# Kernel optimization log

Measured on AMD Instinct MI355X. Metric: run time of the kernel, lower is better.

## Reference

```python
import jax, jax.numpy as jnp
import numpy as np

FP8_MAX = 448.0   # torch.finfo(float8_e4m3fn).max
BLK = 128         # block_size = [128, 128] for weights; [1, 128] for activations
E, H, I, T, TOPK = 8, 2048, 1408, 512, 2
FP8 = jnp.float8_e4m3fn


def fp8_round(x):
    """Round-trip through float8_e4m3fn (simulates .to(float8_e4m3fn))."""
    return jnp.clip(x, -FP8_MAX, FP8_MAX).astype(FP8).astype(jnp.float32)


def setup_inputs() -> dict:
    key = jax.random.key(0)
    ks = jax.random.split(key, 7)
    hidden_states = jax.random.normal(ks[0], (T, H), jnp.float32)
    top_k_index = jax.random.randint(ks[1], (T, TOPK), 0, E)
    top_k_weights = jax.random.uniform(ks[2], (T, TOPK), jnp.float32)
    # FP8 weight codes (stored as fp32 values exactly representable in e4m3fn)
    gate_up_proj = fp8_round(jax.random.normal(ks[3], (E, 2 * I, H), jnp.float32))
    gate_up_proj_scale_inv = jax.random.uniform(ks[4], (E, (2 * I) // BLK, H // BLK), jnp.float32, 1e-4, 1e-2)
    down_proj = fp8_round(jax.random.normal(ks[5], (E, H, I), jnp.float32))
    down_proj_scale_inv = jax.random.uniform(ks[6], (E, H // BLK, I // BLK), jnp.float32, 1e-4, 1e-2)
    return {
        "hidden_states": hidden_states,
        "top_k_index": top_k_index,
        "top_k_weights": top_k_weights,
        "gate_up_proj": gate_up_proj,
        "gate_up_proj_scale_inv": gate_up_proj_scale_inv,
        "down_proj": down_proj,
        "down_proj_scale_inv": down_proj_scale_inv,
    }


def dequant_weight(wq, s):
    # wq: [E, N, K] fp8 codes; s: [E, N//BLK, K//BLK] per-128x128-block scale_inv
    e, n, k = wq.shape
    wb = wq.reshape(e, n // BLK, BLK, k // BLK, BLK)
    return (wb * s[:, :, None, :, None]).reshape(e, n, k)


def quant_dequant_act(x):
    # dynamic per-(row, 128-block) fp8 activation quantization, then dequant
    shp = x.shape
    xb = x.reshape(shp[:-1] + (shp[-1] // BLK, BLK))
    amax = jnp.max(jnp.abs(xb), axis=-1, keepdims=True)
    scale = jnp.maximum(amax, 1e-12) / FP8_MAX
    q = fp8_round(xb / scale)
    return (q * scale).reshape(shp)


def reference(hidden_states, top_k_index, top_k_weights, gate_up_proj,
              gate_up_proj_scale_inv, down_proj, down_proj_scale_inv):
    w_gu = dequant_weight(gate_up_proj, gate_up_proj_scale_inv)  # [E, 2I, H]
    w_d = dequant_weight(down_proj, down_proj_scale_inv)         # [E, H, I]
    # activation quantization is per-token-block, so unrouted tokens are
    # unaffected; dense per-expert compute + combine-weight mask equals the
    # original gather/scatter loop exactly (unrouted contributions weight 0).
    x = quant_dequant_act(hidden_states)                         # [T, H]
    gate_up = jnp.einsum('th,enh->etn', x, w_gu)                 # [E, T, 2I]
    gate, up = jnp.split(gate_up, 2, axis=-1)
    h = jax.nn.silu(gate) * up                                   # [E, T, I]
    h = quant_dequant_act(h)
    down = jnp.einsum('eti,ehi->eth', h, w_d)                    # [E, T, H]
    # combine[t, e] = sum over top-k slots routing token t to expert e
    combine = jnp.sum(jax.nn.one_hot(top_k_index, E, dtype=top_k_weights.dtype)
                      * top_k_weights[..., None], axis=1)        # [T, E]
    out = jnp.einsum('eth,te->th', down, combine)
    return out.astype(hidden_states.dtype)
```

## Files before the change

kernel.cpp:

```cpp
#include <hip/hip_runtime.h>
#include <math.h>

#define NE 8
#define HD 2048
#define ID 1408
#define NT 512
#define NENT 1024
#define FP8MAX 448.0f

typedef __attribute__((ext_vector_type(4))) float floatx4;

__device__ __forceinline__ floatx4 fzero4() {
    floatx4 z; z.x = 0.f; z.y = 0.f; z.z = 0.f; z.w = 0.f; return z;
}

#define OFF_OFFS  0
#define OFF_TOK   1024
#define OFF_WGT   8192
#define OFF_XS    16384
#define OFF_XQ    65536
#define OFF_HS    (2*1024*1024)
#define OFF_HQ    (2*1024*1024 + 65536)
#define OFF_H32   (4*1024*1024)

#define LDA 136

__global__ void route_kernel(const int* __restrict__ tki,
                             const float* __restrict__ tkw,
                             int* __restrict__ offs,
                             int* __restrict__ tok,
                             float* __restrict__ wgt) {
    __shared__ int cnt[NE];
    __shared__ int cur[NE];
    __shared__ int base[NE + 1];
    int tid = threadIdx.x;
    if (tid < NE) { cnt[tid] = 0; cur[tid] = 0; }
    __syncthreads();
    int e = tki[tid];
    atomicAdd(&cnt[e], 1);
    __syncthreads();
    if (tid == 0) {
        int s = 0;
        for (int i = 0; i < NE; i++) { base[i] = s; s += cnt[i]; }
        base[NE] = s;
    }
    __syncthreads();
    int pos = atomicAdd(&cur[e], 1);
    int j = base[e] + pos;
    tok[j] = tid >> 1;
    wgt[j] = tkw[tid];
    if (tid <= NE) offs[tid] = base[tid];
}

__global__ void quant_x_kernel(const float* __restrict__ x,
                               unsigned char* __restrict__ xq,
                               float* __restrict__ xs) {
    int wid = (blockIdx.x * 256 + threadIdx.x) >> 6;
    int lane = threadIdx.x & 63;
    int t = wid >> 4;
    int b = wid & 15;
    const float2 v = *(const float2*)(x + (long)t * HD + b * 128 + lane * 2);
    float am = fmaxf(fabsf(v.x), fabsf(v.y));
    #pragma unroll
    for (int m = 32; m; m >>= 1) am = fmaxf(am, __shfl_xor(am, m));
    float scale = fmaxf(am, 1e-12f) / FP8MAX;
    int p = __builtin_amdgcn_cvt_pk_fp8_f32(v.x / scale, v.y / scale, 0, false);
    *(unsigned short*)(xq + (long)t * HD + b * 128 + lane * 2) =
        (unsigned short)(p & 0xffff);
    if (lane == 0) xs[t * 16 + b] = scale;
}

__global__ void quant_h_kernel(const float* __restrict__ h32,
                               unsigned char* __restrict__ hq,
                               float* __restrict__ hs) {
    int wid = (blockIdx.x * 256 + threadIdx.x) >> 6;
    int lane = threadIdx.x & 63;
    int j = wid / 11;
    int b = wid - j * 11;
    const float2 v = *(const float2*)(h32 + (long)j * ID + b * 128 + lane * 2);
    float am = fmaxf(fabsf(v.x), fabsf(v.y));
    #pragma unroll
    for (int m = 32; m; m >>= 1) am = fmaxf(am, __shfl_xor(am, m));
    float scale = fmaxf(am, 1e-12f) / FP8MAX;
    int p = __builtin_amdgcn_cvt_pk_fp8_f32(v.x / scale, v.y / scale, 0, false);
    *(unsigned short*)(hq + (long)j * ID + b * 128 + lane * 2) =
        (unsigned short)(p & 0xffff);
    if (lane == 0) hs[j * 11 + b] = scale;
}

__global__ __launch_bounds__(256) void gemm1_kernel(
    const unsigned char* __restrict__ xq,
    const float* __restrict__ xs,
    const float* __restrict__ wgu,
    const float* __restrict__ sgu,
    const int* __restrict__ offs,
    const int* __restrict__ tok,
    float* __restrict__ h32) {
    int e = blockIdx.z;
    int mt = blockIdx.y;
    int jb = blockIdx.x;
    int o0 = offs[e], o1 = offs[e + 1];
    int ne = o1 - o0;
    int m0 = mt * 256;
    if (m0 >= ne) return;
    int rem = ne - m0;

    __shared__ __align__(16) unsigned char Asm[256 * LDA];
    __shared__ __align__(16) unsigned char Bsm[64 * LDA];
    __shared__ float sxa[256 * 16];
    __shared__ int tokL[256];

    int tid = threadIdx.x;
    {
        int j = o0 + m0 + tid;
        if (j >= o1) j = o0;
        tokL[tid] = tok[j];
    }
    __syncthreads();
    {
        const float4* s = (const float4*)(xs + tokL[tid] * 16);
        float4 a0 = s[0], a1 = s[1], a2 = s[2], a3 = s[3];
        float4* d = (float4*)(sxa + tid * 16);
        d[0] = a0; d[1] = a1; d[2] = a2; d[3] = a3;
    }

    int wave = tid >> 6;
    int lane = tid & 63;
    int lr = lane & 15;
    int lq = lane >> 4;

    const unsigned char* aptr = xq + (long)tokL[tid] * HD;
    int br = tid >> 2, bq = tid & 3;
    long bn = (br < 32) ? (long)(jb * 32 + br)
                        : (long)(1408 + jb * 32 + (br - 32));
    const float* bptr = wgu + ((long)e * 2816 + bn) * 2048;
    const float* sgp = sgu + (e * 22 + (jb >> 2)) * 16;
    const float* sup = sgu + (e * 22 + 11 + (jb >> 2)) * 16;

    floatx4 facc[16];
    #pragma unroll
    for (int i = 0; i < 16; i++) facc[i] = fzero4();

    for (int kb = 0; kb < 16; kb++) {
        {
            const uint4* src = (const uint4*)(aptr + kb * 128);
            uint4 av[8];
            #pragma unroll
            for (int i = 0; i < 8; i++) av[i] = src[i];
            #pragma unroll
            for (int i = 0; i < 8; i++)
                *(uint4*)(&Asm[tid * LDA + i * 16]) = av[i];
        }
        {
            const float4* src = (const float4*)(bptr + kb * 128 + bq * 32);
            unsigned int pk[8];
            #pragma unroll
            for (int g = 0; g < 8; g++) {
                float4 f = src[g];
                int p = __builtin_amdgcn_cvt_pk_fp8_f32(f.x, f.y, 0, false);
                p = __builtin_amdgcn_cvt_pk_fp8_f32(f.z, f.w, p, true);
                pk[g] = (unsigned int)p;
            }
            *(uint4*)(&Bsm[br * LDA + bq * 32]) =
                make_uint4(pk[0], pk[1], pk[2], pk[3]);
            *(uint4*)(&Bsm[br * LDA + bq * 32 + 16]) =
                make_uint4(pk[4], pk[5], pk[6], pk[7]);
        }
        __syncthreads();
        floatx4 cacc[16];
        #pragma unroll
        for (int i = 0; i < 16; i++) cacc[i] = fzero4();
        #pragma unroll
        for (int ks = 0; ks < 4; ks++) {
            long a[4], b[4];
            #pragma unroll
            for (int mi = 0; mi < 4; mi++)
                a[mi] = *(const long*)(&Asm[(wave * 64 + mi * 16 + lr) * LDA + ks * 32 + lq * 8]);
            #pragma unroll
            for (int ni = 0; ni < 4; ni++)
                b[ni] = *(const long*)(&Bsm[(ni * 16 + lr) * LDA + ks * 32 + lq * 8]);
            #pragma unroll
            for (int mi = 0; mi < 4; mi++)
                #pragma unroll
                for (int ni = 0; ni < 4; ni++)
                    cacc[mi * 4 + ni] = __builtin_amdgcn_mfma_f32_16x16x32_fp8_fp8(
                        a[mi], b[ni], cacc[mi * 4 + ni], 0, 0, 0);
        }
        float sg = sgp[kb];
        float su = sup[kb];
        #pragma unroll
        for (int mi = 0; mi < 4; mi++) {
            #pragma unroll
            for (int reg = 0; reg < 4; reg++) {
                float sx = sxa[(wave * 64 + mi * 16 + lq * 4 + reg) * 16 + kb];
                #pragma unroll
                for (int ni = 0; ni < 4; ni++) {
                    float sw = (ni < 2) ? sg : su;
                    facc[mi * 4 + ni][reg] += cacc[mi * 4 + ni][reg] * (sw * sx);
                }
            }
        }
        __syncthreads();
    }

    #pragma unroll
    for (int mi = 0; mi < 4; mi++) {
        #pragma unroll
        for (int ni = 0; ni < 2; ni++) {
            #pragma unroll
            for (int reg = 0; reg < 4; reg++) {
                int r = wave * 64 + mi * 16 + lq * 4 + reg;
                if (r < rem) {
                    float g = facc[mi * 4 + ni][reg];
                    float u = facc[mi * 4 + ni + 2][reg];
                    float hval = (g / (1.0f + expf(-g))) * u;
                    h32[(long)(o0 + m0 + r) * ID + jb * 32 + ni * 16 + lr] = hval;
                }
            }
        }
    }
}

__global__ __launch_bounds__(256) void gemm2_kernel(
    const unsigned char* __restrict__ hq,
    const float* __restrict__ hs,
    const float* __restrict__ wd,
    const float* __restrict__ sd,
    const int* __restrict__ offs,
    const int* __restrict__ tok,
    const float* __restrict__ wgt,
    float* __restrict__ out) {
    int e = blockIdx.z;
    int mt = blockIdx.y;
    int jb = blockIdx.x;
    int o0 = offs[e], o1 = offs[e + 1];
    int ne = o1 - o0;
    int m0 = mt * 256;
    if (m0 >= ne) return;
    int rem = ne - m0;

    __shared__ __align__(16) unsigned char Asm[256 * LDA];
    __shared__ __align__(16) unsigned char Bsm[64 * LDA];
    __shared__ float sha[256 * 12];
    __shared__ int tokL[256];
    __shared__ float wgtL[256];

    int tid = threadIdx.x;
    int jent;
    {
        int j = o0 + m0 + tid;
        int valid = j < o1;
        if (!valid) j = o0;
        jent = j;
        tokL[tid] = tok[j];
        wgtL[tid] = valid ? wgt[j] : 0.0f;
    }
    {
        const float* s = hs + jent * 11;
        #pragma unroll
        for (int k = 0; k < 11; k++) sha[tid * 12 + k] = s[k];
    }

    int wave = tid >> 6;
    int lane = tid & 63;
    int lr = lane & 15;
    int lq = lane >> 4;

    const unsigned char* aptr = hq + (long)jent * ID;
    int br = tid >> 2, bq = tid & 3;
    const float* bptr = wd + ((long)e * 2048 + jb * 64 + br) * 1408;
    const float* sdp = sd + (e * 16 + (jb >> 1)) * 11;

    floatx4 facc[16];
    #pragma unroll
    for (int i = 0; i < 16; i++) facc[i] = fzero4();

    for (int kb = 0; kb < 11; kb++) {
        {
            const uint4* src = (const uint4*)(aptr + kb * 128);
            uint4 av[8];
            #pragma unroll
            for (int i = 0; i < 8; i++) av[i] = src[i];
            #pragma unroll
            for (int i = 0; i < 8; i++)
                *(uint4*)(&Asm[tid * LDA + i * 16]) = av[i];
        }
        {
            const float4* src = (const float4*)(bptr + kb * 128 + bq * 32);
            unsigned int pk[8];
            #pragma unroll
            for (int g = 0; g < 8; g++) {
                float4 f = src[g];
                int p = __builtin_amdgcn_cvt_pk_fp8_f32(f.x, f.y, 0, false);
                p = __builtin_amdgcn_cvt_pk_fp8_f32(f.z, f.w, p, true);
                pk[g] = (unsigned int)p;
            }
            *(uint4*)(&Bsm[br * LDA + bq * 32]) =
                make_uint4(pk[0], pk[1], pk[2], pk[3]);
            *(uint4*)(&Bsm[br * LDA + bq * 32 + 16]) =
                make_uint4(pk[4], pk[5], pk[6], pk[7]);
        }
        __syncthreads();
        floatx4 cacc[16];
        #pragma unroll
        for (int i = 0; i < 16; i++) cacc[i] = fzero4();
        #pragma unroll
        for (int ks = 0; ks < 4; ks++) {
            long a[4], b[4];
            #pragma unroll
            for (int mi = 0; mi < 4; mi++)
                a[mi] = *(const long*)(&Asm[(wave * 64 + mi * 16 + lr) * LDA + ks * 32 + lq * 8]);
            #pragma unroll
            for (int ni = 0; ni < 4; ni++)
                b[ni] = *(const long*)(&Bsm[(ni * 16 + lr) * LDA + ks * 32 + lq * 8]);
            #pragma unroll
            for (int mi = 0; mi < 4; mi++)
                #pragma unroll
                for (int ni = 0; ni < 4; ni++)
                    cacc[mi * 4 + ni] = __builtin_amdgcn_mfma_f32_16x16x32_fp8_fp8(
                        a[mi], b[ni], cacc[mi * 4 + ni], 0, 0, 0);
        }
        float sw = sdp[kb];
        #pragma unroll
        for (int mi = 0; mi < 4; mi++) {
            #pragma unroll
            for (int reg = 0; reg < 4; reg++) {
                float sh = sha[(wave * 64 + mi * 16 + lq * 4 + reg) * 12 + kb];
                #pragma unroll
                for (int ni = 0; ni < 4; ni++)
                    facc[mi * 4 + ni][reg] += cacc[mi * 4 + ni][reg] * (sw * sh);
            }
        }
        __syncthreads();
    }

    #pragma unroll
    for (int mi = 0; mi < 4; mi++) {
        #pragma unroll
        for (int ni = 0; ni < 4; ni++) {
            #pragma unroll
            for (int reg = 0; reg < 4; reg++) {
                int r = wave * 64 + mi * 16 + lq * 4 + reg;
                if (r < rem) {
                    float v = facc[mi * 4 + ni][reg] * wgtL[r];
                    atomicAdd(out + (long)tokL[r] * HD + jb * 64 + ni * 16 + lr, v);
                }
            }
        }
    }
}

extern "C" void kernel_launch(void* const* d_in, const int* in_sizes, int n_in,
                              void* d_out, int out_size, void* d_ws, size_t ws_size,
                              hipStream_t stream) {
    (void)in_sizes; (void)n_in; (void)out_size; (void)ws_size;
    const float* x   = (const float*)d_in[0];
    const int*   tki = (const int*)d_in[1];
    const float* tkw = (const float*)d_in[2];
    const float* wgu = (const float*)d_in[3];
    const float* sgu = (const float*)d_in[4];
    const float* wd  = (const float*)d_in[5];
    const float* sd  = (const float*)d_in[6];
    float* out = (float*)d_out;
    char* ws = (char*)d_ws;

    int*   offs = (int*)(ws + OFF_OFFS);
    int*   tok  = (int*)(ws + OFF_TOK);
    float* wgt  = (float*)(ws + OFF_WGT);
    float* xs   = (float*)(ws + OFF_XS);
    unsigned char* xq = (unsigned char*)(ws + OFF_XQ);
    float* hs   = (float*)(ws + OFF_HS);
    unsigned char* hq = (unsigned char*)(ws + OFF_HQ);
    float* h32  = (float*)(ws + OFF_H32);

    hipMemsetAsync(d_out, 0, (size_t)NT * HD * sizeof(float), stream);
    route_kernel<<<1, 1024, 0, stream>>>(tki, tkw, offs, tok, wgt);
    quant_x_kernel<<<2048, 256, 0, stream>>>(x, xq, xs);
    gemm1_kernel<<<dim3(44, 4, NE), 256, 0, stream>>>(xq, xs, wgu, sgu, offs, tok, h32);
    quant_h_kernel<<<2816, 256, 0, stream>>>(h32, hq, hs);
    gemm2_kernel<<<dim3(32, 4, NE), 256, 0, stream>>>(hq, hs, wd, sd, offs, tok, wgt, out);
}
```

Measured before the change: 423.7 us.

## Pre-convert fp32 weights to fp8 once per call and prefetch next K tile

```diff
diff --git a/kernel.cpp b/kernel.cpp
--- a/kernel.cpp
+++ b/kernel.cpp
@@ -22,6 +22,9 @@
 #define OFF_HS    (2*1024*1024)
 #define OFF_HQ    (2*1024*1024 + 65536)
 #define OFF_H32   (4*1024*1024)
+#define OFF_WGU8  (10*1024*1024)
+#define OFF_WD8   (OFF_WGU8 + 46137344)
+#define WS_NEED   ((size_t)OFF_WD8 + 23068672)
 
 #define LDA 136
 
@@ -52,6 +55,25 @@
     if (tid <= NE) offs[tid] = base[tid];
 }
 
+__global__ __launch_bounds__(256) void conv_w_kernel(
+    const float* __restrict__ wgu, const float* __restrict__ wd,
+    unsigned char* __restrict__ wgu8, unsigned char* __restrict__ wd8) {
+    const long N1 = 11534336;
+    const long N2 = 5767168;
+    long stride = (long)gridDim.x * 256;
+    for (long i = (long)blockIdx.x * 256 + threadIdx.x; i < N1 + N2; i += stride) {
+        const float4* src;
+        unsigned char* dst;
+        long j;
+        if (i < N1) { src = (const float4*)wgu; dst = wgu8; j = i; }
+        else        { src = (const float4*)wd;  dst = wd8;  j = i - N1; }
+        float4 f = src[j];
+        int p = __builtin_amdgcn_cvt_pk_fp8_f32(f.x, f.y, 0, false);
+        p = __builtin_amdgcn_cvt_pk_fp8_f32(f.z, f.w, p, true);
+        *(unsigned int*)(dst + j * 4) = (unsigned int)p;
+    }
+}
+
 __global__ void quant_x_kernel(const float* __restrict__ x,
                                unsigned char* __restrict__ xq,
                                float* __restrict__ xs) {
@@ -88,10 +110,11 @@
     if (lane == 0) hs[j * 11 + b] = scale;
 }
 
+template<int WFP8>
 __global__ __launch_bounds__(256) void gemm1_kernel(
     const unsigned char* __restrict__ xq,
     const float* __restrict__ xs,
-    const float* __restrict__ wgu,
+    const void* __restrict__ wguv,
     const float* __restrict__ sgu,
     const int* __restrict__ offs,
     const int* __restrict__ tok,
@@ -133,7 +156,8 @@
     int br = tid >> 2, bq = tid & 3;
     long bn = (br < 32) ? (long)(jb * 32 + br)
                         : (long)(1408 + jb * 32 + (br - 32));
-    const float* bptr = wgu + ((long)e * 2816 + bn) * 2048;
+    const unsigned char* bptr8 = WFP8 ? (const unsigned char*)wguv + ((long)e * 2816 + bn) * 2048 : nullptr;
+    const float* bptrf = WFP8 ? nullptr : (const float*)wguv + ((long)e * 2816 + bn) * 2048;
     const float* sgp = sgu + (e * 22 + (jb >> 2)) * 16;
     const float* sup = sgu + (e * 22 + 11 + (jb >> 2)) * 16;
 
@@ -141,22 +165,38 @@
     #pragma unroll
     for (int i = 0; i < 16; i++) facc[i] = fzero4();
 
+    uint4 aP[8];
+    uint4 bP8[2];
+    float4 bPf[8];
+
+    auto loadAB = [&](int kb) {
+        const uint4* asrc = (const uint4*)(aptr + kb * 128);
+        #pragma unroll
+        for (int i = 0; i < 8; i++) aP[i] = asrc[i];
+        if (WFP8) {
+            const uint4* bsrc = (const uint4*)(bptr8 + kb * 128 + bq * 32);
+            bP8[0] = bsrc[0];
+            bP8[1] = bsrc[1];
+        } else {
+            const float4* bsrc = (const float4*)(bptrf + kb * 128 + bq * 32);
+            #pragma unroll
+            for (int g = 0; g < 8; g++) bPf[g] = bsrc[g];
+        }
+    };
+    loadAB(0);
+
     for (int kb = 0; kb < 16; kb++) {
-        {
-            const uint4* src = (const uint4*)(aptr + kb * 128);
-            uint4 av[8];
-            #pragma unroll
-            for (int i = 0; i < 8; i++) av[i] = src[i];
-            #pragma unroll
-            for (int i = 0; i < 8; i++)
-                *(uint4*)(&Asm[tid * LDA + i * 16]) = av[i];
-        }
-        {
-            const float4* src = (const float4*)(bptr + kb * 128 + bq * 32);
+        #pragma unroll
+        for (int i = 0; i < 8; i++)
+            *(uint4*)(&Asm[tid * LDA + i * 16]) = aP[i];
+        if (WFP8) {
+            *(uint4*)(&Bsm[br * LDA + bq * 32]) = bP8[0];
+            *(uint4*)(&Bsm[br * LDA + bq * 32 + 16]) = bP8[1];
+        } else {
             unsigned int pk[8];
             #pragma unroll
             for (int g = 0; g < 8; g++) {
-                float4 f = src[g];
+                float4 f = bPf[g];
                 int p = __builtin_amdgcn_cvt_pk_fp8_f32(f.x, f.y, 0, false);
                 p = __builtin_amdgcn_cvt_pk_fp8_f32(f.z, f.w, p, true);
                 pk[g] = (unsigned int)p;
@@ -167,6 +207,7 @@
                 make_uint4(pk[4], pk[5], pk[6], pk[7]);
         }
         __syncthreads();
+        if (kb < 15) loadAB(kb + 1);
         floatx4 cacc[16];
         #pragma unroll
         for (int i = 0; i < 16; i++) cacc[i] = fzero4();
@@ -221,10 +262,11 @@
     }
 }
 
+template<int WFP8>
 __global__ __launch_bounds__(256) void gemm2_kernel(
     const unsigned char* __restrict__ hq,
     const float* __restrict__ hs,
-    const float* __restrict__ wd,
+    const void* __restrict__ wdv,
     const float* __restrict__ sd,
     const int* __restrict__ offs,
     const int* __restrict__ tok,
@@ -268,29 +310,46 @@
 
     const unsigned char* aptr = hq + (long)jent * ID;
     int br = tid >> 2, bq = tid & 3;
-    const float* bptr = wd + ((long)e * 2048 + jb * 64 + br) * 1408;
+    const unsigned char* bptr8 = WFP8 ? (const unsigned char*)wdv + ((long)e * 2048 + jb * 64 + br) * 1408 : nullptr;
+    const float* bptrf = WFP8 ? nullptr : (const float*)wdv + ((long)e * 2048 + jb * 64 + br) * 1408;
     const float* sdp = sd + (e * 16 + (jb >> 1)) * 11;
 
     floatx4 facc[16];
     #pragma unroll
     for (int i = 0; i < 16; i++) facc[i] = fzero4();
 
+    uint4 aP[8];
+    uint4 bP8[2];
+    float4 bPf[8];
+
+    auto loadAB = [&](int kb) {
+        const uint4* asrc = (const uint4*)(aptr + kb * 128);
+        #pragma unroll
+        for (int i = 0; i < 8; i++) aP[i] = asrc[i];
+        if (WFP8) {
+            const uint4* bsrc = (const uint4*)(bptr8 + kb * 128 + bq * 32);
+            bP8[0] = bsrc[0];
+            bP8[1] = bsrc[1];
+        } else {
+            const float4* bsrc = (const float4*)(bptrf + kb * 128 + bq * 32);
+            #pragma unroll
+            for (int g = 0; g < 8; g++) bPf[g] = bsrc[g];
+        }
+    };
+    loadAB(0);
+
     for (int kb = 0; kb < 11; kb++) {
-        {
-            const uint4* src = (const uint4*)(aptr + kb * 128);
-            uint4 av[8];
-            #pragma unroll
-            for (int i = 0; i < 8; i++) av[i] = src[i];
-            #pragma unroll
-            for (int i = 0; i < 8; i++)
-                *(uint4*)(&Asm[tid * LDA + i * 16]) = av[i];
-        }
-        {
-            const float4* src = (const float4*)(bptr + kb * 128 + bq * 32);
+        #pragma unroll
+        for (int i = 0; i < 8; i++)
+            *(uint4*)(&Asm[tid * LDA + i * 16]) = aP[i];
+        if (WFP8) {
+            *(uint4*)(&Bsm[br * LDA + bq * 32]) = bP8[0];
+            *(uint4*)(&Bsm[br * LDA + bq * 32 + 16]) = bP8[1];
+        } else {
             unsigned int pk[8];
             #pragma unroll
             for (int g = 0; g < 8; g++) {
-                float4 f = src[g];
+                float4 f = bPf[g];
                 int p = __builtin_amdgcn_cvt_pk_fp8_f32(f.x, f.y, 0, false);
                 p = __builtin_amdgcn_cvt_pk_fp8_f32(f.z, f.w, p, true);
                 pk[g] = (unsigned int)p;
@@ -301,6 +360,7 @@
                 make_uint4(pk[4], pk[5], pk[6], pk[7]);
         }
         __syncthreads();
+        if (kb < 10) loadAB(kb + 1);
         floatx4 cacc[16];
         #pragma unroll
         for (int i = 0; i < 16; i++) cacc[i] = fzero4();
@@ -353,7 +413,7 @@
 extern "C" void kernel_launch(void* const* d_in, const int* in_sizes, int n_in,
                               void* d_out, int out_size, void* d_ws, size_t ws_size,
                               hipStream_t stream) {
-    (void)in_sizes; (void)n_in; (void)out_size; (void)ws_size;
+    (void)in_sizes; (void)n_in; (void)out_size;
     const float* x   = (const float*)d_in[0];
     const int*   tki = (const int*)d_in[1];
     const float* tkw = (const float*)d_in[2];
@@ -372,11 +432,22 @@
     float* hs   = (float*)(ws + OFF_HS);
     unsigned char* hq = (unsigned char*)(ws + OFF_HQ);
     float* h32  = (float*)(ws + OFF_H32);
+    unsigned char* wgu8 = (unsigned char*)(ws + OFF_WGU8);
+    unsigned char* wd8  = (unsigned char*)(ws + OFF_WD8);
+
+    bool big = ws_size >= WS_NEED;
 
     hipMemsetAsync(d_out, 0, (size_t)NT * HD * sizeof(float), stream);
     route_kernel<<<1, 1024, 0, stream>>>(tki, tkw, offs, tok, wgt);
     quant_x_kernel<<<2048, 256, 0, stream>>>(x, xq, xs);
-    gemm1_kernel<<<dim3(44, 4, NE), 256, 0, stream>>>(xq, xs, wgu, sgu, offs, tok, h32);
-    quant_h_kernel<<<2816, 256, 0, stream>>>(h32, hq, hs);
-    gemm2_kernel<<<dim3(32, 4, NE), 256, 0, stream>>>(hq, hs, wd, sd, offs, tok, wgt, out);
-}
+    if (big) {
+        conv_w_kernel<<<4096, 256, 0, stream>>>(wgu, wd, wgu8, wd8);
+        gemm1_kernel<1><<<dim3(44, 4, NE), 256, 0, stream>>>(xq, xs, wgu8, sgu, offs, tok, h32);
+        quant_h_kernel<<<2816, 256, 0, stream>>>(h32, hq, hs);
+        gemm2_kernel<1><<<dim3(32, 4, NE), 256, 0, stream>>>(hq, hs, wd8, sd, offs, tok, wgt, out);
+    } else {
+        gemm1_kernel<0><<<dim3(44, 4, NE), 256, 0, stream>>>(xq, xs, wgu, sgu, offs, tok, h32);
+        quant_h_kernel<<<2816, 256, 0, stream>>>(h32, hq, hs);
+        gemm2_kernel<0><<<dim3(32, 4, NE), 256, 0, stream>>>(hq, hs, wd, sd, offs, tok, wgt, out);
+    }
+}
```

Measured after the change: 562.8 us. 1.33x slower.

## Pre-gather routed activations, shrink GEMM M-tiles, and prefetch next K-block into registers

Applied to the files above, without the earlier changes.

```diff
diff --git a/kernel.cpp b/kernel.cpp
--- a/kernel.cpp
+++ b/kernel.cpp
@@ -5,7 +5,6 @@
 #define HD 2048
 #define ID 1408
 #define NT 512
-#define NENT 1024
 #define FP8MAX 448.0f
 
 typedef __attribute__((ext_vector_type(4))) float floatx4;
@@ -17,11 +16,12 @@
 #define OFF_OFFS  0
 #define OFF_TOK   1024
 #define OFF_WGT   8192
-#define OFF_XS    16384
-#define OFF_XQ    65536
-#define OFF_HS    (2*1024*1024)
-#define OFF_HQ    (2*1024*1024 + 65536)
-#define OFF_H32   (4*1024*1024)
+#define OFF_ENT   16384
+#define OFF_XSG   32768
+#define OFF_XG    131072
+#define OFF_HS    (3*1024*1024)
+#define OFF_HQ    (3*1024*1024 + 65536)
+#define OFF_H32   (5*1024*1024)
 
 #define LDA 136
 
@@ -29,7 +29,8 @@
                              const float* __restrict__ tkw,
                              int* __restrict__ offs,
                              int* __restrict__ tok,
-                             float* __restrict__ wgt) {
+                             float* __restrict__ wgt,
+                             int* __restrict__ ent) {
     __shared__ int cnt[NE];
     __shared__ int cur[NE];
     __shared__ int base[NE + 1];
@@ -49,12 +50,14 @@
     int j = base[e] + pos;
     tok[j] = tid >> 1;
     wgt[j] = tkw[tid];
+    ent[tid] = j;
     if (tid <= NE) offs[tid] = base[tid];
 }
 
 __global__ void quant_x_kernel(const float* __restrict__ x,
-                               unsigned char* __restrict__ xq,
-                               float* __restrict__ xs) {
+                               const int* __restrict__ ent,
+                               unsigned char* __restrict__ xg,
+                               float* __restrict__ xsg) {
     int wid = (blockIdx.x * 256 + threadIdx.x) >> 6;
     int lane = threadIdx.x & 63;
     int t = wid >> 4;
@@ -65,9 +68,11 @@
     for (int m = 32; m; m >>= 1) am = fmaxf(am, __shfl_xor(am, m));
     float scale = fmaxf(am, 1e-12f) / FP8MAX;
     int p = __builtin_amdgcn_cvt_pk_fp8_f32(v.x / scale, v.y / scale, 0, false);
-    *(unsigned short*)(xq + (long)t * HD + b * 128 + lane * 2) =
-        (unsigned short)(p & 0xffff);
-    if (lane == 0) xs[t * 16 + b] = scale;
+    unsigned short pk = (unsigned short)(p & 0xffff);
+    int e0 = ent[2 * t], e1 = ent[2 * t + 1];
+    *(unsigned short*)(xg + (long)e0 * HD + b * 128 + lane * 2) = pk;
+    *(unsigned short*)(xg + (long)e1 * HD + b * 128 + lane * 2) = pk;
+    if (lane == 0) { xsg[e0 * 16 + b] = scale; xsg[e1 * 16 + b] = scale; }
 }
 
 __global__ void quant_h_kernel(const float* __restrict__ h32,
@@ -89,39 +94,34 @@
 }
 
 __global__ __launch_bounds__(256) void gemm1_kernel(
-    const unsigned char* __restrict__ xq,
-    const float* __restrict__ xs,
+    const unsigned char* __restrict__ xg,
+    const float* __restrict__ xsg,
     const float* __restrict__ wgu,
     const float* __restrict__ sgu,
     const int* __restrict__ offs,
-    const int* __restrict__ tok,
     float* __restrict__ h32) {
     int e = blockIdx.z;
     int mt = blockIdx.y;
     int jb = blockIdx.x;
     int o0 = offs[e], o1 = offs[e + 1];
     int ne = o1 - o0;
-    int m0 = mt * 256;
+    int m0 = mt * 128;
     if (m0 >= ne) return;
     int rem = ne - m0;
-
-    __shared__ __align__(16) unsigned char Asm[256 * LDA];
+    int j0 = o0 + m0;
+
+    __shared__ __align__(16) unsigned char Asm[128 * LDA];
     __shared__ __align__(16) unsigned char Bsm[64 * LDA];
-    __shared__ float sxa[256 * 16];
-    __shared__ int tokL[256];
+    __shared__ float sxa[128 * 20];
 
     int tid = threadIdx.x;
     {
-        int j = o0 + m0 + tid;
-        if (j >= o1) j = o0;
-        tokL[tid] = tok[j];
-    }
-    __syncthreads();
-    {
-        const float4* s = (const float4*)(xs + tokL[tid] * 16);
-        float4 a0 = s[0], a1 = s[1], a2 = s[2], a3 = s[3];
-        float4* d = (float4*)(sxa + tid * 16);
-        d[0] = a0; d[1] = a1; d[2] = a2; d[3] = a3;
+        int r = tid >> 1, q = tid & 1;
+        int j = j0 + r; if (j >= o1) j = o0;
+        float4 s0 = *(const float4*)(xsg + j * 16 + q * 8);
+        float4 s1 = *(const float4*)(xsg + j * 16 + q * 8 + 4);
+        *(float4*)&sxa[r * 20 + q * 8] = s0;
+        *(float4*)&sxa[r * 20 + q * 8 + 4] = s1;
     }
 
     int wave = tid >> 6;
@@ -129,34 +129,49 @@
     int lr = lane & 15;
     int lq = lane >> 4;
 
-    const unsigned char* aptr = xq + (long)tokL[tid] * HD;
+    const unsigned char* aRow[4];
+    int aseg = tid & 7;
+    int arow[4];
+    #pragma unroll
+    for (int s = 0; s < 4; s++) {
+        int r = s * 32 + (tid >> 3);
+        arow[s] = r;
+        int j = j0 + r; if (j >= o1) j = o0;
+        aRow[s] = xg + (long)j * HD + aseg * 16;
+    }
+
     int br = tid >> 2, bq = tid & 3;
     long bn = (br < 32) ? (long)(jb * 32 + br)
                         : (long)(1408 + jb * 32 + (br - 32));
-    const float* bptr = wgu + ((long)e * 2816 + bn) * 2048;
+    const float* bptr = wgu + ((long)e * 2816 + bn) * HD;
     const float* sgp = sgu + (e * 22 + (jb >> 2)) * 16;
     const float* sup = sgu + (e * 22 + 11 + (jb >> 2)) * 16;
 
-    floatx4 facc[16];
-    #pragma unroll
-    for (int i = 0; i < 16; i++) facc[i] = fzero4();
+    floatx4 facc[8];
+    #pragma unroll
+    for (int i = 0; i < 8; i++) facc[i] = fzero4();
+
+    uint4 aP[4];
+    float4 bPf[8];
+    auto loadAB = [&](int kb) {
+        #pragma unroll
+        for (int s = 0; s < 4; s++)
+            aP[s] = *(const uint4*)(aRow[s] + kb * 128);
+        const float4* bsrc = (const float4*)(bptr + kb * 128 + bq * 32);
+        #pragma unroll
+        for (int g = 0; g < 8; g++) bPf[g] = bsrc[g];
+    };
+    loadAB(0);
 
     for (int kb = 0; kb < 16; kb++) {
+        #pragma unroll
+        for (int s = 0; s < 4; s++)
+            *(uint4*)(&Asm[arow[s] * LDA + aseg * 16]) = aP[s];
         {
-            const uint4* src = (const uint4*)(aptr + kb * 128);
-            uint4 av[8];
-            #pragma unroll
-            for (int i = 0; i < 8; i++) av[i] = src[i];
-            #pragma unroll
-            for (int i = 0; i < 8; i++)
-                *(uint4*)(&Asm[tid * LDA + i * 16]) = av[i];
-        }
-        {
-            const float4* src = (const float4*)(bptr + kb * 128 + bq * 32);
             unsigned int pk[8];
             #pragma unroll
             for (int g = 0; g < 8; g++) {
-                float4 f = src[g];
+                float4 f = bPf[g];
                 int p = __builtin_amdgcn_cvt_pk_fp8_f32(f.x, f.y, 0, false);
                 p = __builtin_amdgcn_cvt_pk_fp8_f32(f.z, f.w, p, true);
                 pk[g] = (unsigned int)p;
@@ -167,20 +182,21 @@
                 make_uint4(pk[4], pk[5], pk[6], pk[7]);
         }
         __syncthreads();
-        floatx4 cacc[16];
-        #pragma unroll
-        for (int i = 0; i < 16; i++) cacc[i] = fzero4();
+        if (kb < 15) loadAB(kb + 1);
+        floatx4 cacc[8];
+        #pragma unroll
+        for (int i = 0; i < 8; i++) cacc[i] = fzero4();
         #pragma unroll
         for (int ks = 0; ks < 4; ks++) {
-            long a[4], b[4];
-            #pragma unroll
-            for (int mi = 0; mi < 4; mi++)
-                a[mi] = *(const long*)(&Asm[(wave * 64 + mi * 16 + lr) * LDA + ks * 32 + lq * 8]);
+            long a[2], b[4];
+            #pragma unroll
+            for (int mi = 0; mi < 2; mi++)
+                a[mi] = *(const long*)(&Asm[(wave * 32 + mi * 16 + lr) * LDA + ks * 32 + lq * 8]);
             #pragma unroll
             for (int ni = 0; ni < 4; ni++)
                 b[ni] = *(const long*)(&Bsm[(ni * 16 + lr) * LDA + ks * 32 + lq * 8]);
             #pragma unroll
-            for (int mi = 0; mi < 4; mi++)
+            for (int mi = 0; mi < 2; mi++)
                 #pragma unroll
                 for (int ni = 0; ni < 4; ni++)
                     cacc[mi * 4 + ni] = __builtin_amdgcn_mfma_f32_16x16x32_fp8_fp8(
@@ -189,10 +205,10 @@
         float sg = sgp[kb];
         float su = sup[kb];
         #pragma unroll
-        for (int mi = 0; mi < 4; mi++) {
+        for (int mi = 0; mi < 2; mi++) {
             #pragma unroll
             for (int reg = 0; reg < 4; reg++) {
-                float sx = sxa[(wave * 64 + mi * 16 + lq * 4 + reg) * 16 + kb];
+                float sx = sxa[(wave * 32 + mi * 16 + lq * 4 + reg) * 20 + kb];
                 #pragma unroll
                 for (int ni = 0; ni < 4; ni++) {
                     float sw = (ni < 2) ? sg : su;
@@ -204,17 +220,17 @@
     }
 
     #pragma unroll
-    for (int mi = 0; mi < 4; mi++) {
+    for (int mi = 0; mi < 2; mi++) {
         #pragma unroll
         for (int ni = 0; ni < 2; ni++) {
             #pragma unroll
             for (int reg = 0; reg < 4; reg++) {
-                int r = wave * 64 + mi * 16 + lq * 4 + reg;
+                int r = wave * 32 + mi * 16 + lq * 4 + reg;
                 if (r < rem) {
                     float g = facc[mi * 4 + ni][reg];
                     float u = facc[mi * 4 + ni + 2][reg];
                     float hval = (g / (1.0f + expf(-g))) * u;
-                    h32[(long)(o0 + m0 + r) * ID + jb * 32 + ni * 16 + lr] = hval;
+                    h32[(long)(j0 + r) * ID + jb * 32 + ni * 16 + lr] = hval;
                 }
             }
         }
@@ -235,28 +251,25 @@
     int jb = blockIdx.x;
     int o0 = offs[e], o1 = offs[e + 1];
     int ne = o1 - o0;
-    int m0 = mt * 256;
+    int m0 = mt * 128;
     if (m0 >= ne) return;
     int rem = ne - m0;
-
-    __shared__ __align__(16) unsigned char Asm[256 * LDA];
-    __shared__ __align__(16) unsigned char Bsm[64 * LDA];
-    __shared__ float sha[256 * 12];
-    __shared__ int tokL[256];
-    __shared__ float wgtL[256];
+    int j0 = o0 + m0;
+
+    __shared__ __align__(16) unsigned char Asm[128 * LDA];
+    __shared__ __align__(16) unsigned char Bsm[32 * LDA];
+    __shared__ float sha[128 * 12];
+    __shared__ int tokL[128];
+    __shared__ float wgtL[128];
 
     int tid = threadIdx.x;
-    int jent;
-    {
-        int j = o0 + m0 + tid;
+    if (tid < 128) {
+        int j = j0 + tid;
         int valid = j < o1;
         if (!valid) j = o0;
-        jent = j;
         tokL[tid] = tok[j];
         wgtL[tid] = valid ? wgt[j] : 0.0f;
-    }
-    {
-        const float* s = hs + jent * 11;
+        const float* s = hs + j * 11;
         #pragma unroll
         for (int k = 0; k < 11; k++) sha[tid * 12 + k] = s[k];
     }
@@ -266,84 +279,98 @@
     int lr = lane & 15;
     int lq = lane >> 4;
 
-    const unsigned char* aptr = hq + (long)jent * ID;
-    int br = tid >> 2, bq = tid & 3;
-    const float* bptr = wd + ((long)e * 2048 + jb * 64 + br) * 1408;
-    const float* sdp = sd + (e * 16 + (jb >> 1)) * 11;
-
-    floatx4 facc[16];
-    #pragma unroll
-    for (int i = 0; i < 16; i++) facc[i] = fzero4();
+    const unsigned char* aRow[4];
+    int aseg = tid & 7;
+    int arow[4];
+    #pragma unroll
+    for (int s = 0; s < 4; s++) {
+        int r = s * 32 + (tid >> 3);
+        arow[s] = r;
+        int j = j0 + r; if (j >= o1) j = o0;
+        aRow[s] = hq + (long)j * ID + aseg * 16;
+    }
+
+    int br = tid >> 3, bq = tid & 7;
+    const float* bptr = wd + ((long)e * HD + jb * 32 + br) * ID;
+    const float* sdp = sd + (e * 16 + (jb >> 2)) * 11;
+
+    floatx4 facc[4];
+    #pragma unroll
+    for (int i = 0; i < 4; i++) facc[i] = fzero4();
+
+    uint4 aP[4];
+    float4 bPf[4];
+    auto loadAB = [&](int kb) {
+        #pragma unroll
+        for (int s = 0; s < 4; s++)
+            aP[s] = *(const uint4*)(aRow[s] + kb * 128);
+        const float4* bsrc = (const float4*)(bptr + kb * 128 + bq * 16);
+        #pragma unroll
+        for (int g = 0; g < 4; g++) bPf[g] = bsrc[g];
+    };
+    loadAB(0);
 
     for (int kb = 0; kb < 11; kb++) {
+        #pragma unroll
+        for (int s = 0; s < 4; s++)
+            *(uint4*)(&Asm[arow[s] * LDA + aseg * 16]) = aP[s];
         {
-            const uint4* src = (const uint4*)(aptr + kb * 128);
-            uint4 av[8];
-            #pragma unroll
-            for (int i = 0; i < 8; i++) av[i] = src[i];
-            #pragma unroll
-            for (int i = 0; i < 8; i++)
-                *(uint4*)(&Asm[tid * LDA + i * 16]) = av[i];
-        }
-        {
-            const float4* src = (const float4*)(bptr + kb * 128 + bq * 32);
-            unsigned int pk[8];
-            #pragma unroll
-            for (int g = 0; g < 8; g++) {
-                float4 f = src[g];
+            unsigned int pk[4];
+            #pragma unroll
+            for (int g = 0; g < 4; g++) {
+                float4 f = bPf[g];
                 int p = __builtin_amdgcn_cvt_pk_fp8_f32(f.x, f.y, 0, false);
                 p = __builtin_amdgcn_cvt_pk_fp8_f32(f.z, f.w, p, true);
                 pk[g] = (unsigned int)p;
             }
-            *(uint4*)(&Bsm[br * LDA + bq * 32]) =
+            *(uint4*)(&Bsm[br * LDA + bq * 16]) =
                 make_uint4(pk[0], pk[1], pk[2], pk[3]);
-            *(uint4*)(&Bsm[br * LDA + bq * 32 + 16]) =
-                make_uint4(pk[4], pk[5], pk[6], pk[7]);
         }
         __syncthreads();
-        floatx4 cacc[16];
-        #pragma unroll
-        for (int i = 0; i < 16; i++) cacc[i] = fzero4();
+        if (kb < 10) loadAB(kb + 1);
+        floatx4 cacc[4];
+        #pragma unroll
+        for (int i = 0; i < 4; i++) cacc[i] = fzero4();
         #pragma unroll
         for (int ks = 0; ks < 4; ks++) {
-            long a[4], b[4];
-            #pragma unroll
-            for (int mi = 0; mi < 4; mi++)
-                a[mi] = *(const long*)(&Asm[(wave * 64 + mi * 16 + lr) * LDA + ks * 32 + lq * 8]);
-            #pragma unroll
-            for (int ni = 0; ni < 4; ni++)
+            long a[2], b[2];
+            #pragma unroll
+            for (int mi = 0; mi < 2; mi++)
+                a[mi] = *(const long*)(&Asm[(wave * 32 + mi * 16 + lr) * LDA + ks * 32 + lq * 8]);
+            #pragma unroll
+            for (int ni = 0; ni < 2; ni++)
                 b[ni] = *(const long*)(&Bsm[(ni * 16 + lr) * LDA + ks * 32 + lq * 8]);
             #pragma unroll
-            for (int mi = 0; mi < 4; mi++)
+            for (int mi = 0; mi < 2; mi++)
                 #pragma unroll
-                for (int ni = 0; ni < 4; ni++)
-                    cacc[mi * 4 + ni] = __builtin_amdgcn_mfma_f32_16x16x32_fp8_fp8(
-                        a[mi], b[ni], cacc[mi * 4 + ni], 0, 0, 0);
+                for (int ni = 0; ni < 2; ni++)
+                    cacc[mi * 2 + ni] = __builtin_amdgcn_mfma_f32_16x16x32_fp8_fp8(
+                        a[mi], b[ni], cacc[mi * 2 + ni], 0, 0, 0);
         }
         float sw = sdp[kb];
         #pragma unroll
-        for (int mi = 0; mi < 4; mi++) {
+        for (int mi = 0; mi < 2; mi++) {
             #pragma unroll
             for (int reg = 0; reg < 4; reg++) {
-                float sh = sha[(wave * 64 + mi * 16 + lq * 4 + reg) * 12 + kb];
+                float sh = sha[(wave * 32 + mi * 16 + lq * 4 + reg) * 12 + kb];
                 #pragma unroll
-                for (int ni = 0; ni < 4; ni++)
-                    facc[mi * 4 + ni][reg] += cacc[mi * 4 + ni][reg] * (sw * sh);
+                for (int ni = 0; ni < 2; ni++)
+                    facc[mi * 2 + ni][reg] += cacc[mi * 2 + ni][reg] * (sw * sh);
             }
         }
         __syncthreads();
     }
 
     #pragma unroll
-    for (int mi = 0; mi < 4; mi++) {
-        #pragma unroll
-        for (int ni = 0; ni < 4; ni++) {
+    for (int mi = 0; mi < 2; mi++) {
+        #pragma unroll
+        for (int ni = 0; ni < 2; ni++) {
             #pragma unroll
             for (int reg = 0; reg < 4; reg++) {
-                int r = wave * 64 + mi * 16 + lq * 4 + reg;
+                int r = wave * 32 + mi * 16 + lq * 4 + reg;
                 if (r < rem) {
-                    float v = facc[mi * 4 + ni][reg] * wgtL[r];
-                    atomicAdd(out + (long)tokL[r] * HD + jb * 64 + ni * 16 + lr, v);
+                    float v = facc[mi * 2 + ni][reg] * wgtL[r];
+                    atomicAdd(out + (long)tokL[r] * HD + jb * 32 + ni * 16 + lr, v);
                 }
             }
         }
@@ -367,16 +394,17 @@
     int*   offs = (int*)(ws + OFF_OFFS);
     int*   tok  = (int*)(ws + OFF_TOK);
     float* wgt  = (float*)(ws + OFF_WGT);
-    float* xs   = (float*)(ws + OFF_XS);
-    unsigned char* xq = (unsigned char*)(ws + OFF_XQ);
+    int*   ent  = (int*)(ws + OFF_ENT);
+    float* xsg  = (float*)(ws + OFF_XSG);
+    unsigned char* xg = (unsigned char*)(ws + OFF_XG);
     float* hs   = (float*)(ws + OFF_HS);
     unsigned char* hq = (unsigned char*)(ws + OFF_HQ);
     float* h32  = (float*)(ws + OFF_H32);
 
     hipMemsetAsync(d_out, 0, (size_t)NT * HD * sizeof(float), stream);
-    route_kernel<<<1, 1024, 0, stream>>>(tki, tkw, offs, tok, wgt);
-    quant_x_kernel<<<2048, 256, 0, stream>>>(x, xq, xs);
-    gemm1_kernel<<<dim3(44, 4, NE), 256, 0, stream>>>(xq, xs, wgu, sgu, offs, tok, h32);
+    route_kernel<<<1, 1024, 0, stream>>>(tki, tkw, offs, tok, wgt, ent);
+    quant_x_kernel<<<2048, 256, 0, stream>>>(x, ent, xg, xsg);
+    gemm1_kernel<<<dim3(44, 8, NE), 256, 0, stream>>>(xg, xsg, wgu, sgu, offs, h32);
     quant_h_kernel<<<2816, 256, 0, stream>>>(h32, hq, hs);
-    gemm2_kernel<<<dim3(32, 4, NE), 256, 0, stream>>>(hq, hs, wd, sd, offs, tok, wgt, out);
-}
+    gemm2_kernel<<<dim3(64, 8, NE), 256, 0, stream>>>(hq, hs, wd, sd, offs, tok, wgt, out);
+}
```

Result: slower. 477.6 us (+12.7%).
